# Kernel optimization log

Hardware: AMD Instinct MI355X
Metric: run time of the kernel (lower is better)

The kernel has to match this reference:

```python
import jax, jax.numpy as jnp
import numpy as np

V, D, T, H, L, B = 50257, 1024, 1024, 16, 6, 2
HS = D // H  # 64
EPS = 1e-5


def setup_inputs() -> dict:
    key = jax.random.key(0)
    ks = jax.random.split(key, 16)
    s = 0.02
    n = lambda k, sh: jax.random.normal(k, sh, jnp.float32) * s
    return {
        'idx': jax.random.randint(ks[0], (B, T), 0, V),
        'targets': jax.random.randint(ks[1], (B, T), 0, V),
        'tok_emb': n(ks[2], (V, D)),
        'pos_emb': n(ks[3], (T, D)),
        'wq': n(ks[4], (L, H, D, HS)),
        'wk': n(ks[5], (L, H, D, HS)),
        'wv': n(ks[6], (L, H, D, HS)),
        'wproj': n(ks[7], (L, D, D)),
        'bproj': jnp.zeros((L, D), jnp.float32),
        'ln1_g': jnp.ones((L, D), jnp.float32),
        'ln1_b': jnp.zeros((L, D), jnp.float32),
        'ln2_g': jnp.ones((L, D), jnp.float32),
        'ln2_b': jnp.zeros((L, D), jnp.float32),
        'w1': n(ks[8], (L, D, 4 * D)),
        'b1': jnp.zeros((L, 4 * D), jnp.float32),
        'w2': n(ks[9], (L, 4 * D, D)),
        'b2': jnp.zeros((L, D), jnp.float32),
        'lnf_g': jnp.ones((D,), jnp.float32),
        'lnf_b': jnp.zeros((D,), jnp.float32),
        'lm_w': n(ks[10], (D, V)),
        'lm_b': jnp.zeros((V,), jnp.float32),
    }


def _layernorm(x, g, b):
    mu = jnp.mean(x, axis=-1, keepdims=True)
    var = jnp.var(x, axis=-1, keepdims=True)
    return (x - mu) * jax.lax.rsqrt(var + EPS) * g + b


def _forward(idx, targets, tok_emb, pos_emb, wq, wk, wv, wproj, bproj,
             ln1_g, ln1_b, ln2_g, ln2_b, w1, b1, w2, b2, lnf_g, lnf_b, lm_w, lm_b):
    t = idx.shape[1]
    x = tok_emb[idx] + pos_emb[:t]  # [B,T,D]
    causal = jnp.tril(jnp.ones((t, t), bool))  # [T,T]
    neg_inf = jnp.float32(-jnp.inf)

    def block(x, p):
        (wq_l, wk_l, wv_l, wp_l, bp_l, g1, b1_ln, g2, b2_ln, wf1, bf1, wf2, bf2) = p
        h = _layernorm(x, g1, b1_ln)
        q = jnp.einsum('btd,hdk->bhtk', h, wq_l)
        k = jnp.einsum('btd,hdk->bhtk', h, wk_l)
        v = jnp.einsum('btd,hdk->bhtk', h, wv_l)
        scores = jnp.einsum('bhtk,bhsk->bhts', q, k) * (HS ** -0.5)
        scores = jnp.where(causal, scores, neg_inf)
        attn = jax.nn.softmax(scores, axis=-1)  # dropout p=0.0
        o = jnp.einsum('bhts,bhsk->bhtk', attn, v)
        o = o.transpose(0, 2, 1, 3).reshape(x.shape[0], t, H * HS)  # concat heads
        x = x + o @ wp_l + bp_l
        h2 = _layernorm(x, g2, b2_ln)
        x = x + jax.nn.relu(h2 @ wf1 + bf1) @ wf2 + bf2
        return x, None

    x, _ = jax.lax.scan(block, x, (wq, wk, wv, wproj, bproj,
                                   ln1_g, ln1_b, ln2_g, ln2_b, w1, b1, w2, b2))
    x = _layernorm(x, lnf_g, lnf_b)
    logits = x @ lm_w + lm_b  # [B,T,V]
    logp = jax.nn.log_softmax(logits, axis=-1)
    loss = -jnp.mean(jnp.take_along_axis(logp, targets[..., None], axis=-1))
    return logits, loss


def reference(idx, targets, tok_emb, pos_emb, wq, wk, wv, wproj, bproj,
              ln1_g, ln1_b, ln2_g, ln2_b, w1, b1, w2, b2, lnf_g, lnf_b, lm_w, lm_b):
    return _forward(idx, targets, tok_emb, pos_emb, wq, wk, wv, wproj, bproj,
                    ln1_g, ln1_b, ln2_g, ln2_b, w1, b1, w2, b2, lnf_g, lnf_b, lm_w, lm_b)
```

## Files before the change

kernel.cpp:

```cpp
#include <hip/hip_runtime.h>
#include <cstdint>
#include <cstddef>

typedef unsigned short u16;
typedef unsigned int u32;
typedef __bf16 bf16x8 __attribute__((ext_vector_type(8)));
typedef float f32x4 __attribute__((ext_vector_type(4)));
typedef short short8_t __attribute__((ext_vector_type(8)));

#define NV 50257
#define NVPAD 50304
#define ND 1024
#define NT 1024
#define NH 16
#define NL 6
#define NB 2
#define NM 2048
#define NF 4096
#define EPSLN 1e-5f

__device__ __forceinline__ u16 f2bf(float f) {
    unsigned u = __float_as_uint(f);
    return (u16)((u + 0x7fffu + ((u >> 16) & 1u)) >> 16);
}
__device__ __forceinline__ float bf2f(u16 h) {
    return __uint_as_float(((unsigned)h) << 16);
}
__device__ __forceinline__ u32 pack2bf(float lo, float hi) {
    return (u32)f2bf(lo) | ((u32)f2bf(hi) << 16);
}

__device__ __forceinline__ void gload_lds16(const u16* g, u16* l) {
    __builtin_amdgcn_global_load_lds((const __attribute__((address_space(1))) void*)g,
                                     (__attribute__((address_space(3))) void*)l, 16, 0, 0);
}

__device__ __forceinline__ float wave_reduce_sum(float v) {
#pragma unroll
    for (int off = 32; off >= 1; off >>= 1) v += __shfl_xor(v, off, 64);
    return v;
}

__global__ __launch_bounds__(256) void k_embed(const int* __restrict__ idx,
                                               const float* __restrict__ tok,
                                               const float* __restrict__ pos,
                                               float* __restrict__ x) {
    int m = blockIdx.x;
    int t = m & (NT - 1);
    int tokid = idx[m];
    int d = threadIdx.x * 4;
    float4 a = *(const float4*)(tok + (size_t)tokid * ND + d);
    float4 p = *(const float4*)(pos + (size_t)t * ND + d);
    a.x += p.x; a.y += p.y; a.z += p.z; a.w += p.w;
    *(float4*)(x + (size_t)m * ND + d) = a;
}

__global__ __launch_bounds__(256) void k_layernorm(const float* __restrict__ x,
                                                   const float* __restrict__ g,
                                                   const float* __restrict__ b,
                                                   u16* __restrict__ outb) {
    int m = blockIdx.x;
    int d = threadIdx.x * 4;
    const float4 v = *(const float4*)(x + (size_t)m * ND + d);
    float s = v.x + v.y + v.z + v.w;
    float q = v.x * v.x + v.y * v.y + v.z * v.z + v.w * v.w;
    s = wave_reduce_sum(s);
    q = wave_reduce_sum(q);
    __shared__ float ss[4], sq[4];
    int lane = threadIdx.x & 63, w = threadIdx.x >> 6;
    if (lane == 0) { ss[w] = s; sq[w] = q; }
    __syncthreads();
    s = ss[0] + ss[1] + ss[2] + ss[3];
    q = sq[0] + sq[1] + sq[2] + sq[3];
    float mu = s * (1.0f / ND);
    float var = q * (1.0f / ND) - mu * mu;
    float rstd = rsqrtf(var + EPSLN);
    float4 gg = *(const float4*)(g + d);
    float4 bb = *(const float4*)(b + d);
    ushort4 pk;
    pk.x = f2bf((v.x - mu) * rstd * gg.x + bb.x);
    pk.y = f2bf((v.y - mu) * rstd * gg.y + bb.y);
    pk.z = f2bf((v.z - mu) * rstd * gg.z + bb.z);
    pk.w = f2bf((v.w - mu) * rstd * gg.w + bb.w);
    *(ushort4*)(outb + (size_t)m * ND + d) = pk;
}

__global__ __launch_bounds__(256) void k_wtrans(const float* __restrict__ W,
                                                u16* __restrict__ Wt,
                                                int K, int N, int Npad, int hs, int ld) {
    __shared__ float t[32][33];
    const int nb = blockIdx.x << 5, kb = blockIdx.y << 5;
    const int tx = threadIdx.x & 31, tq = threadIdx.x >> 5;
    const int n = nb + tx;
    if (n < N) {
        const int head = n / hs, nc = n - head * hs;
        const float* src = W + (size_t)head * K * hs + nc;
#pragma unroll
        for (int i = 0; i < 4; ++i)
            t[(tq << 2) + i][tx] = src[(size_t)(kb + (tq << 2) + i) * ld];
    } else {
#pragma unroll
        for (int i = 0; i < 4; ++i) t[(tq << 2) + i][tx] = 0.f;
    }
    __syncthreads();
#pragma unroll
    for (int i = 0; i < 4; ++i) {
        const int nn = nb + (tq << 2) + i;
        if (nn < Npad) Wt[(size_t)nn * K + kb + tx] = f2bf(t[tx][(tq << 2) + i]);
    }
}

__global__ __launch_bounds__(256) void k_wtrans_qkv(const float* __restrict__ Wq,
                                                    const float* __restrict__ Wk,
                                                    const float* __restrict__ Wv,
                                                    u16* __restrict__ Wt) {
    __shared__ float t[32][33];
    const float* W = (blockIdx.z == 0) ? Wq : (blockIdx.z == 1) ? Wk : Wv;
    u16* dst = Wt + (size_t)blockIdx.z * ND * ND;
    const int nb = blockIdx.x << 5, kb = blockIdx.y << 5;
    const int tx = threadIdx.x & 31, tq = threadIdx.x >> 5;
    const int n = nb + tx;
    {
        const int head = n >> 6, nc = n & 63;
        const float* src = W + (size_t)head * ND * 64 + nc;
#pragma unroll
        for (int i = 0; i < 4; ++i)
            t[(tq << 2) + i][tx] = src[(size_t)(kb + (tq << 2) + i) * 64];
    }
    __syncthreads();
#pragma unroll
    for (int i = 0; i < 4; ++i) {
        const int nn = nb + (tq << 2) + i;
        dst[(size_t)nn * ND + kb + tx] = f2bf(t[tx][(tq << 2) + i]);
    }
}

__global__ __launch_bounds__(256) void k_vtrans(const u16* __restrict__ qkv,
                                                u16* __restrict__ vt) {
    __shared__ u16 L[64][72];
    const int tt = blockIdx.x, bh = blockIdx.y;
    const int b = bh >> 4, h = bh & 15;
    const int tid = threadIdx.x;
    const int tr = tid >> 2, dc = (tid & 3) << 4;
    const u16* src = qkv + (size_t)(b * NT + tt * 64 + tr) * 3072 + 2048 + h * 64 + dc;
    short8_t v0 = *(const short8_t*)src;
    short8_t v1 = *(const short8_t*)(src + 8);
#pragma unroll
    for (int j = 0; j < 8; ++j) { L[tr][dc + j] = (u16)v0[j]; L[tr][dc + 8 + j] = (u16)v1[j]; }
    __syncthreads();
    const int dr = tid >> 2, tc = (tid & 3) << 4;
    union { u16 us[16]; short8_t v[2]; } tmp;
#pragma unroll
    for (int j = 0; j < 16; ++j) tmp.us[j] = L[tc + j][dr];
    u16* dst = vt + ((size_t)bh * 64 + dr) * NT + tt * 64 + tc;
    *(short8_t*)dst = tmp.v[0];
    *(short8_t*)(dst + 8) = tmp.v[1];
}

__global__ __launch_bounds__(512) void k_gemm_lm(
    const u16* __restrict__ A, const u16* __restrict__ Bt,
    const float* __restrict__ bias,
    float* __restrict__ Cf,
    int K, int N, int ldc)
{
    __shared__ u16 As[2][256 * 32];
    __shared__ u16 Bs[2][128 * 32];
    const int lin = blockIdx.y * 8 + blockIdx.x;
    const int nwg = (int)gridDim.y * 8;
    const int cpx = nwg >> 3;
    const int swz = (lin & 7) * cpx + (lin >> 3);
    const int m0 = (swz & 7) * 256;
    const int n0 = (swz >> 3) * 128;
    const int tid = threadIdx.x;
    const int lane = tid & 63, w = tid >> 6;
    const int wr = w >> 1, wc = w & 1;
    const int lr = lane & 15, kg = lane >> 4;

    const int srow = lane >> 2;
    const int scol = (((lane & 3) ^ ((lane >> 3) & 3)) << 3);
    const u16* gA0 = A + (size_t)(m0 + w * 16 + srow) * K + scol;
    const u16* gA1 = gA0 + (size_t)128 * K;
    const u16* gB0 = Bt + (size_t)(n0 + w * 16 + srow) * K + scol;

    f32x4 acc[4][4] = {};
    const int nt = K >> 5;

    gload_lds16(gA0, &As[0][w * 512]);
    gload_lds16(gA1, &As[0][4096 + w * 512]);
    gload_lds16(gB0, &Bs[0][w * 512]);
    __syncthreads();

    int cur = 0;
    for (int t = 0; t < nt; ++t) {
        if (t + 1 < nt) {
            const int ko = (t + 1) << 5;
            gload_lds16(gA0 + ko, &As[cur ^ 1][w * 512]);
            gload_lds16(gA1 + ko, &As[cur ^ 1][4096 + w * 512]);
            gload_lds16(gB0 + ko, &Bs[cur ^ 1][w * 512]);
        }
        bf16x8 af[4], bfr[4];
        const int rsw = ((kg ^ ((lr >> 1) & 3)) << 3);
#pragma unroll
        for (int mi = 0; mi < 4; ++mi)
            af[mi] = *(const bf16x8*)&As[cur][(wr * 64 + mi * 16 + lr) * 32 + rsw];
#pragma unroll
        for (int ni = 0; ni < 4; ++ni)
            bfr[ni] = *(const bf16x8*)&Bs[cur][(wc * 64 + ni * 16 + lr) * 32 + rsw];
#pragma unroll
        for (int mi = 0; mi < 4; ++mi)
#pragma unroll
            for (int ni = 0; ni < 4; ++ni)
                acc[mi][ni] = __builtin_amdgcn_mfma_f32_16x16x32_bf16(af[mi], bfr[ni], acc[mi][ni], 0, 0, 0);
        __syncthreads();
        cur ^= 1;
    }
#pragma unroll
    for (int mi = 0; mi < 4; ++mi)
#pragma unroll
        for (int ni = 0; ni < 4; ++ni)
#pragma unroll
            for (int r = 0; r < 4; ++r) {
                const int row = m0 + wr * 64 + mi * 16 + kg * 4 + r;
                const int col = n0 + wc * 64 + ni * 16 + lr;
                if (col >= N) continue;
                Cf[(size_t)row * ldc + col] = acc[mi][ni][r] + bias[col];
            }
}

template <bool RELU, bool NBOUND, bool OUTBF16>
__global__ __launch_bounds__(256) void k_mfma_gemm(
    const u16* __restrict__ A, const u16* __restrict__ Bt,
    const float* __restrict__ bias,
    float* __restrict__ Cf, u16* __restrict__ Cb,
    int K, int N, int ldc)
{
    __shared__ u16 As[2][128 * 32];
    __shared__ u16 Bs[2][128 * 32];
    const int lin = blockIdx.y * 16 + blockIdx.x;
    const int nwg = (int)gridDim.y * 16;
    const int cpx = nwg >> 3;
    const int swz = (lin & 7) * cpx + (lin >> 3);
    const int m0 = (swz & 15) * 128;
    const int n0 = (swz >> 4) * 128;
    const int tid = threadIdx.x;
    const int lane = tid & 63, wv = tid >> 6;
    const int wr = wv >> 1, wc = wv & 1;
    const int lr = lane & 15, kg = lane >> 4;

    const int srow = lane >> 2;
    const int scol = (((lane & 3) ^ ((lane >> 3) & 3)) << 3);
    const u16* gA0 = A + (size_t)(m0 + wv * 16 + srow) * K + scol;
    const u16* gA1 = gA0 + (size_t)64 * K;
    const u16* gB0 = Bt + (size_t)(n0 + wv * 16 + srow) * K + scol;
    const u16* gB1 = gB0 + (size_t)64 * K;

    f32x4 acc[4][4] = {};
    const int nt = K >> 5;

    gload_lds16(gA0, &As[0][wv * 512]);
    gload_lds16(gA1, &As[0][2048 + wv * 512]);
    gload_lds16(gB0, &Bs[0][wv * 512]);
    gload_lds16(gB1, &Bs[0][2048 + wv * 512]);
    __syncthreads();

    int cur = 0;
    for (int t = 0; t < nt; ++t) {
        if (t + 1 < nt) {
            const int ko = (t + 1) << 5;
            gload_lds16(gA0 + ko, &As[cur ^ 1][wv * 512]);
            gload_lds16(gA1 + ko, &As[cur ^ 1][2048 + wv * 512]);
            gload_lds16(gB0 + ko, &Bs[cur ^ 1][wv * 512]);
            gload_lds16(gB1 + ko, &Bs[cur ^ 1][2048 + wv * 512]);
        }
        bf16x8 af[4], bfr[4];
        const int rsw = ((kg ^ ((lr >> 1) & 3)) << 3);
#pragma unroll
        for (int mi = 0; mi < 4; ++mi) {
            const int R = wr * 64 + mi * 16 + lr;
            af[mi] = *(const bf16x8*)&As[cur][R * 32 + rsw];
        }
#pragma unroll
        for (int ni = 0; ni < 4; ++ni) {
            const int R = wc * 64 + ni * 16 + lr;
            bfr[ni] = *(const bf16x8*)&Bs[cur][R * 32 + rsw];
        }
#pragma unroll
        for (int mi = 0; mi < 4; ++mi)
#pragma unroll
            for (int ni = 0; ni < 4; ++ni)
                acc[mi][ni] = __builtin_amdgcn_mfma_f32_16x16x32_bf16(af[mi], bfr[ni], acc[mi][ni], 0, 0, 0);
        __syncthreads();
        cur ^= 1;
    }
#pragma unroll
    for (int mi = 0; mi < 4; ++mi) {
#pragma unroll
        for (int ni = 0; ni < 4; ++ni) {
#pragma unroll
            for (int r = 0; r < 4; ++r) {
                const int row = m0 + wr * 64 + mi * 16 + kg * 4 + r;
                const int col = n0 + wc * 64 + ni * 16 + lr;
                if (NBOUND && col >= N) continue;
                float c = acc[mi][ni][r];
                if (bias) c += bias[col];
                if (RELU) c = fmaxf(c, 0.f);
                if (OUTBF16) Cb[(size_t)row * ldc + col] = f2bf(c);
                else         Cf[(size_t)row * ldc + col] = c;
            }
        }
    }
}

template <bool RELU, bool RESID, bool OUTBF16>
__global__ __launch_bounds__(256) void k_gemm_n64(
    const u16* __restrict__ A, const u16* __restrict__ Bt,
    const float* __restrict__ bias, const float* __restrict__ resid,
    float* __restrict__ Cf, u16* __restrict__ Cb,
    int K, int ldc)
{
    __shared__ u16 As[2][128 * 32];
    __shared__ u16 Bs[2][64 * 32];
    const int lin = blockIdx.y * 16 + blockIdx.x;
    const int nwg = (int)gridDim.y * 16;
    const int cpx = nwg >> 3;
    const int swz = (lin & 7) * cpx + (lin >> 3);
    const int m0 = (swz & 15) * 128;
    const int n0 = (swz >> 4) * 64;
    const int tid = threadIdx.x;
    const int lane = tid & 63, wv = tid >> 6;
    const int lr = lane & 15, kg = lane >> 4;

    const int srow = lane >> 2;
    const int scol = (((lane & 3) ^ ((lane >> 3) & 3)) << 3);
    const u16* gA0 = A + (size_t)(m0 + wv * 32 + srow) * K + scol;
    const u16* gA1 = gA0 + (size_t)16 * K;
    const u16* gB0 = Bt + (size_t)(n0 + wv * 16 + srow) * K + scol;

    f32x4 acc[2][4] = {};
    const int nt = K >> 5;

    gload_lds16(gA0, &As[0][wv * 1024]);
    gload_lds16(gA1, &As[0][wv * 1024 + 512]);
    gload_lds16(gB0, &Bs[0][wv * 512]);
    __syncthreads();

    int cur = 0;
    for (int t = 0; t < nt; ++t) {
        if (t + 1 < nt) {
            const int ko = (t + 1) << 5;
            gload_lds16(gA0 + ko, &As[cur ^ 1][wv * 1024]);
            gload_lds16(gA1 + ko, &As[cur ^ 1][wv * 1024 + 512]);
            gload_lds16(gB0 + ko, &Bs[cur ^ 1][wv * 512]);
        }
        bf16x8 af[2], bfr[4];
        const int rsw = ((kg ^ ((lr >> 1) & 3)) << 3);
#pragma unroll
        for (int mi = 0; mi < 2; ++mi)
            af[mi] = *(const bf16x8*)&As[cur][(wv * 32 + mi * 16 + lr) * 32 + rsw];
#pragma unroll
        for (int ni = 0; ni < 4; ++ni)
            bfr[ni] = *(const bf16x8*)&Bs[cur][(ni * 16 + lr) * 32 + rsw];
#pragma unroll
        for (int mi = 0; mi < 2; ++mi)
#pragma unroll
            for (int ni = 0; ni < 4; ++ni)
                acc[mi][ni] = __builtin_amdgcn_mfma_f32_16x16x32_bf16(af[mi], bfr[ni], acc[mi][ni], 0, 0, 0);
        __syncthreads();
        cur ^= 1;
    }
#pragma unroll
    for (int mi = 0; mi < 2; ++mi) {
#pragma unroll
        for (int ni = 0; ni < 4; ++ni) {
#pragma unroll
            for (int r = 0; r < 4; ++r) {
                const int row = m0 + wv * 32 + mi * 16 + kg * 4 + r;
                const int col = n0 + ni * 16 + lr;
                float c = acc[mi][ni][r];
                if (bias) c += bias[col];
                if (RELU) c = fmaxf(c, 0.f);
                if (RESID) c += resid[(size_t)row * ldc + col];
                if (OUTBF16) Cb[(size_t)row * ldc + col] = f2bf(c);
                else         Cf[(size_t)row * ldc + col] = c;
            }
        }
    }
}

__global__ __launch_bounds__(256) void k_attn_mfma(const u16* __restrict__ qkv,
                                                   const u16* __restrict__ vt,
                                                   u16* __restrict__ ob) {
    const int qt = blockIdx.x, bh = blockIdx.y;
    const int b = bh >> 4, h = bh & 15;
    const int tid = threadIdx.x;
    const int lane = tid & 63, w = tid >> 6;
    const int lr = lane & 15, kg = lane >> 4;

    __shared__ u16 Qs[64 * 64];
    __shared__ u16 Ks[2][64 * 64];
    __shared__ u16 Vs[2][64 * 64];

    const int srow8 = lane >> 3;
    const int csw = ((lane & 7) ^ srow8) << 3;

    {
        const int r0 = w * 8 + srow8;
        gload_lds16(qkv + (size_t)(b * NT + qt * 64 + r0) * 3072 + h * 64 + csw, &Qs[w * 512]);
        gload_lds16(qkv + (size_t)(b * NT + qt * 64 + 32 + r0) * 3072 + h * 64 + csw, &Qs[2048 + w * 512]);
    }
#define STAGE_KV(bb, st)                                                                            \
    {                                                                                               \
        const int r0_ = w * 8 + srow8;                                                              \
        gload_lds16(qkv + (size_t)(b * NT + (st) * 64 + r0_) * 3072 + 1024 + h * 64 + csw,          \
                    &Ks[bb][w * 512]);                                                              \
        gload_lds16(qkv + (size_t)(b * NT + (st) * 64 + 32 + r0_) * 3072 + 1024 + h * 64 + csw,     \
                    &Ks[bb][2048 + w * 512]);                                                       \
        gload_lds16(vt + ((size_t)bh * 64 + r0_) * NT + (st) * 64 + csw, &Vs[bb][w * 512]);         \
        gload_lds16(vt + ((size_t)bh * 64 + 32 + r0_) * NT + (st) * 64 + csw,                       \
                    &Vs[bb][2048 + w * 512]);                                                       \
    }
    STAGE_KV(0, 0);
    __syncthreads();

    bf16x8 qf[2];
    {
        const int qrow = w * 16 + lr;
#pragma unroll
        for (int ds_ = 0; ds_ < 2; ++ds_)
            qf[ds_] = *(const bf16x8*)&Qs[qrow * 64 + ((((ds_ << 2) + kg) ^ (lr & 7)) << 3)];
    }

    float mstate = -3.0e38f, lstate = 0.f;
    f32x4 acc_o[4] = {};
    const int qg = qt * 64 + w * 16 + lr;

    int cur = 0;
    for (int st = 0; st <= qt; ++st) {
        if (st < qt) STAGE_KV(cur ^ 1, st + 1);
        const bool diag = (st == qt);
        const int milim = diag ? w : 3;

        f32x4 acc_s[4] = {};
#pragma unroll
        for (int mi = 0; mi < 4; ++mi) {
            if (mi <= milim) {
                const int srw = mi * 16 + lr;
#pragma unroll
                for (int ds_ = 0; ds_ < 2; ++ds_) {
                    bf16x8 kf = *(const bf16x8*)&Ks[cur][srw * 64 + ((((ds_ << 2) + kg) ^ (lr & 7)) << 3)];
                    acc_s[mi] = __builtin_amdgcn_mfma_f32_16x16x32_bf16(kf, qf[ds_], acc_s[mi], 0, 0, 0);
                }
            }
        }
        float tilemax = -3.0e38f;
#pragma unroll
        for (int mi = 0; mi < 4; ++mi)
#pragma unroll
            for (int r = 0; r < 4; ++r) {
                float x_ = acc_s[mi][r] * 0.125f;
                const int sg = st * 64 + mi * 16 + kg * 4 + r;
                if (mi > milim || sg > qg) x_ = -3.0e38f;
                acc_s[mi][r] = x_;
                tilemax = fmaxf(tilemax, x_);
            }
        tilemax = fmaxf(tilemax, __shfl_xor(tilemax, 16));
        tilemax = fmaxf(tilemax, __shfl_xor(tilemax, 32));
        const float mnew = fmaxf(mstate, tilemax);
        const float rfac = __expf(mstate - mnew);
        mstate = mnew;

        float psum = 0.f;
        u32 pk[4][2];
#pragma unroll
        for (int mi = 0; mi < 4; ++mi) {
            float p0 = __expf(acc_s[mi][0] - mnew);
            float p1 = __expf(acc_s[mi][1] - mnew);
            float p2 = __expf(acc_s[mi][2] - mnew);
            float p3 = __expf(acc_s[mi][3] - mnew);
            psum += p0 + p1 + p2 + p3;
            pk[mi][0] = pack2bf(p0, p1);
            pk[mi][1] = pack2bf(p2, p3);
        }
        psum += __shfl_xor(psum, 16);
        psum += __shfl_xor(psum, 32);
        lstate = lstate * rfac + psum;

        float rf[4];
#pragma unroll
        for (int r = 0; r < 4; ++r) rf[r] = __shfl(rfac, kg * 4 + r);
#pragma unroll
        for (int ni = 0; ni < 4; ++ni)
#pragma unroll
            for (int r = 0; r < 4; ++r) acc_o[ni][r] *= rf[r];

        const int src0 = ((kg & 1) << 5) + lr;
        const int src1 = src0 + 16;
#pragma unroll
        for (int ks_ = 0; ks_ < 2; ++ks_) {
            const u32 lo_a = __shfl((int)pk[ks_ * 2][0], src0);
            const u32 lo_b = __shfl((int)pk[ks_ * 2][1], src0);
            const u32 lo_c = __shfl((int)pk[ks_ * 2][0], src1);
            const u32 lo_d = __shfl((int)pk[ks_ * 2][1], src1);
            const u32 hi_a = __shfl((int)pk[ks_ * 2 + 1][0], src0);
            const u32 hi_b = __shfl((int)pk[ks_ * 2 + 1][1], src0);
            const u32 hi_c = __shfl((int)pk[ks_ * 2 + 1][0], src1);
            const u32 hi_d = __shfl((int)pk[ks_ * 2 + 1][1], src1);
            union { u32 u[4]; bf16x8 v; } pa;
            pa.u[0] = (kg & 2) ? hi_a : lo_a;
            pa.u[1] = (kg & 2) ? hi_b : lo_b;
            pa.u[2] = (kg & 2) ? hi_c : lo_c;
            pa.u[3] = (kg & 2) ? hi_d : lo_d;
#pragma unroll
            for (int ni = 0; ni < 4; ++ni) {
                const int drow = ni * 16 + lr;
                bf16x8 vf = *(const bf16x8*)&Vs[cur][drow * 64 + ((((ks_ << 2) + kg) ^ (lr & 7)) << 3)];
                acc_o[ni] = __builtin_amdgcn_mfma_f32_16x16x32_bf16(pa.v, vf, acc_o[ni], 0, 0, 0);
            }
        }
        __syncthreads();
        cur ^= 1;
    }

    float il[4];
#pragma unroll
    for (int r = 0; r < 4; ++r) il[r] = 1.0f / __shfl(lstate, kg * 4 + r);
#pragma unroll
    for (int ni = 0; ni < 4; ++ni)
#pragma unroll
        for (int r = 0; r < 4; ++r) {
            const int q2 = qt * 64 + w * 16 + kg * 4 + r;
            ob[(size_t)(b * NT + q2) * ND + h * 64 + ni * 16 + lr] = f2bf(acc_o[ni][r] * il[r]);
        }
#undef STAGE_KV
}

__global__ __launch_bounds__(256) void k_rowloss(const float* __restrict__ logits,
                                                 const int* __restrict__ targets,
                                                 float* __restrict__ rl) {
    const int m = blockIdx.x;
    const float* row = logits + (size_t)m * NV;
    const int tid = threadIdx.x;
    const int lane = tid & 63, w = tid >> 6;
    const int a = (4 - (m & 3)) & 3;
    const float4* rv = (const float4*)(row + a);
    const int nv4 = (NV - a) >> 2;
    const int tail0 = a + (nv4 << 2);

    float mx = -INFINITY;
    if (tid < a) mx = row[tid];
    for (int j = tid; j < nv4; j += 256) {
        float4 v = rv[j];
        mx = fmaxf(fmaxf(mx, v.x), fmaxf(v.y, fmaxf(v.z, v.w)));
    }
    for (int j = tail0 + tid; j < NV; j += 256) mx = fmaxf(mx, row[j]);
#pragma unroll
    for (int off = 32; off >= 1; off >>= 1) mx = fmaxf(mx, __shfl_xor(mx, off, 64));
    __shared__ float sm[4];
    if (lane == 0) sm[w] = mx;
    __syncthreads();
    mx = fmaxf(fmaxf(sm[0], sm[1]), fmaxf(sm[2], sm[3]));

    float s = 0.f;
    if (tid < a) s += __expf(row[tid] - mx);
    for (int j = tid; j < nv4; j += 256) {
        float4 v = rv[j];
        s += __expf(v.x - mx) + __expf(v.y - mx) + __expf(v.z - mx) + __expf(v.w - mx);
    }
    for (int j = tail0 + tid; j < NV; j += 256) s += __expf(row[j] - mx);
    s = wave_reduce_sum(s);
    __shared__ float sv[4];
    if (lane == 0) sv[w] = s;
    __syncthreads();
    s = sv[0] + sv[1] + sv[2] + sv[3];
    if (tid == 0) {
        float lse = logf(s) + mx;
        rl[m] = lse - row[targets[m]];
    }
}

__global__ __launch_bounds__(256) void k_lossreduce(const float* __restrict__ rl,
                                                    float* __restrict__ out_loss) {
    int tid = threadIdx.x;
    float s = 0.f;
    for (int j = tid; j < NM; j += 256) s += rl[j];
    s = wave_reduce_sum(s);
    __shared__ float sv[4];
    int lane = tid & 63, w = tid >> 6;
    if (lane == 0) sv[w] = s;
    __syncthreads();
    if (tid == 0) out_loss[0] = (sv[0] + sv[1] + sv[2] + sv[3]) * (1.0f / NM);
}

extern "C" void kernel_launch(void* const* d_in, const int* in_sizes, int n_in,
                              void* d_out, int out_size, void* d_ws, size_t ws_size,
                              hipStream_t stream) {
    const int* idx      = (const int*)d_in[0];
    const int* targets  = (const int*)d_in[1];
    const float* tok    = (const float*)d_in[2];
    const float* pos    = (const float*)d_in[3];
    const float* wq     = (const float*)d_in[4];
    const float* wk     = (const float*)d_in[5];
    const float* wv     = (const float*)d_in[6];
    const float* wproj  = (const float*)d_in[7];
    const float* bproj  = (const float*)d_in[8];
    const float* ln1_g  = (const float*)d_in[9];
    const float* ln1_b  = (const float*)d_in[10];
    const float* ln2_g  = (const float*)d_in[11];
    const float* ln2_b  = (const float*)d_in[12];
    const float* w1     = (const float*)d_in[13];
    const float* b1     = (const float*)d_in[14];
    const float* w2     = (const float*)d_in[15];
    const float* b2     = (const float*)d_in[16];
    const float* lnf_g  = (const float*)d_in[17];
    const float* lnf_b  = (const float*)d_in[18];
    const float* lm_w   = (const float*)d_in[19];
    const float* lm_b   = (const float*)d_in[20];
    float* out = (float*)d_out;

    char* wsb = (char*)d_ws;
    auto alloc = [&](size_t bytes) { char* p = wsb; wsb += (bytes + 255) & ~(size_t)255; return p; };
    float* x     = (float*)alloc((size_t)NM * ND * 4);
    u16* h_bf    = (u16*)  alloc((size_t)NM * ND * 2);
    float* rl    = (float*)alloc((size_t)NM * 4);
    char* region = (char*)alloc((size_t)NVPAD * ND * 2);
    u16* qkv_bf = (u16*)(region);
    u16* vt_bf  = (u16*)(region + ((size_t)12 << 20));
    u16* ob_bf  = (u16*)(region + ((size_t)16 << 20));
    u16* hid_bf = (u16*)(region + ((size_t)20 << 20));
    u16* wqkv_t = (u16*)(region + ((size_t)36 << 20));
    u16* wp_t   = (u16*)(region + ((size_t)42 << 20));
    u16* w1_t   = (u16*)(region + ((size_t)44 << 20));
    u16* w2_t   = (u16*)(region + ((size_t)52 << 20));
    u16* lm_t   = (u16*)(region);

    k_embed<<<NM, 256, 0, stream>>>(idx, tok, pos, x);

    for (int l = 0; l < NL; ++l) {
        const float* wq_l = wq + (size_t)l * NH * ND * 64;
        const float* wk_l = wk + (size_t)l * NH * ND * 64;
        const float* wv_l = wv + (size_t)l * NH * ND * 64;
        const float* wp_l = wproj + (size_t)l * ND * ND;
        const float* bp_l = bproj + (size_t)l * ND;
        const float* w1_l = w1 + (size_t)l * ND * NF;
        const float* b1_l = b1 + (size_t)l * NF;
        const float* w2_l = w2 + (size_t)l * NF * ND;
        const float* b2_l = b2 + (size_t)l * ND;

        k_layernorm<<<NM, 256, 0, stream>>>(x, ln1_g + (size_t)l * ND, ln1_b + (size_t)l * ND, h_bf);

        k_wtrans_qkv<<<dim3(32, 32, 3), 256, 0, stream>>>(wq_l, wk_l, wv_l, wqkv_t);
        k_mfma_gemm<false, false, true><<<dim3(16, 24), 256, 0, stream>>>(
            h_bf, wqkv_t, nullptr, nullptr, qkv_bf, ND, 3 * ND, 3 * ND);

        k_vtrans<<<dim3(NT / 64, NB * NH), 256, 0, stream>>>(qkv_bf, vt_bf);
        k_attn_mfma<<<dim3(NT / 64, NB * NH), 256, 0, stream>>>(qkv_bf, vt_bf, ob_bf);

        k_wtrans<<<dim3(ND / 32, ND / 32), 256, 0, stream>>>(wp_l, wp_t, ND, ND, ND, ND, ND);
        k_gemm_n64<false, true, false><<<dim3(16, 16), 256, 0, stream>>>(
            ob_bf, wp_t, bp_l, x, x, nullptr, ND, ND);

        k_layernorm<<<NM, 256, 0, stream>>>(x, ln2_g + (size_t)l * ND, ln2_b + (size_t)l * ND, h_bf);

        k_wtrans<<<dim3(NF / 32, ND / 32), 256, 0, stream>>>(w1_l, w1_t, ND, NF, NF, NF, NF);
        k_mfma_gemm<true, false, true><<<dim3(16, 32), 256, 0, stream>>>(
            h_bf, w1_t, b1_l, nullptr, hid_bf, ND, NF, NF);

        k_wtrans<<<dim3(ND / 32, NF / 32), 256, 0, stream>>>(w2_l, w2_t, NF, ND, ND, ND, ND);
        k_gemm_n64<false, true, false><<<dim3(16, 16), 256, 0, stream>>>(
            hid_bf, w2_t, b2_l, x, x, nullptr, NF, ND);
    }

    k_layernorm<<<NM, 256, 0, stream>>>(x, lnf_g, lnf_b, h_bf);

    k_wtrans<<<dim3(NVPAD / 32, ND / 32), 256, 0, stream>>>(lm_w, lm_t, ND, NV, NVPAD, NV, NV);
    k_gemm_lm<<<dim3(8, NVPAD / 128), 512, 0, stream>>>(
        h_bf, lm_t, lm_b, out, ND, NV, NV);

    k_rowloss<<<NM, 256, 0, stream>>>(out, targets, rl);
    k_lossreduce<<<1, 256, 0, stream>>>(rl, out + (size_t)NM * NV);
}
```

Baseline: 1.894 ms.

## Fuse softmax partials into LM GEMM, split-K the FFN down-projection, reorder attention blocks

The LM-head GEMM epilogue now computes a per-row max and sum-exp for each 128-column tile and writes them to small partial buffers. A light combine kernel reduces these to the loss, so the 400MB logits tensor is no longer reread in a separate row-loss pass. The FFN down-projection is split into two K halves written to a scratch buffer, then summed with bias and residual in a combine kernel, which raises the block count at the cost of extra traffic. Attention reverses the query-tile order for the second batch to balance causal work across blocks.

New measurement: 1.663 ms. 12.2% less time.

```diff
diff --git a/kernel.cpp b/kernel.cpp
--- a/kernel.cpp
+++ b/kernel.cpp
@@ -10,6 +10,7 @@
 
 #define NV 50257
 #define NVPAD 50304
+#define NBLK_LM 393
 #define ND 1024
 #define NT 1024
 #define NH 16
@@ -161,6 +162,7 @@
     const u16* __restrict__ A, const u16* __restrict__ Bt,
     const float* __restrict__ bias,
     float* __restrict__ Cf,
+    float* __restrict__ pmax_g, float* __restrict__ psum_g,
     int K, int N, int ldc)
 {
     __shared__ u16 As[2][256 * 32];
@@ -214,6 +216,7 @@
         __syncthreads();
         cur ^= 1;
     }
+
 #pragma unroll
     for (int mi = 0; mi < 4; ++mi)
 #pragma unroll
@@ -223,8 +226,55 @@
                 const int row = m0 + wr * 64 + mi * 16 + kg * 4 + r;
                 const int col = n0 + wc * 64 + ni * 16 + lr;
                 if (col >= N) continue;
-                Cf[(size_t)row * ldc + col] = acc[mi][ni][r] + bias[col];
+                acc[mi][ni][r] += bias[col];
+                Cf[(size_t)row * ldc + col] = acc[mi][ni][r];
             }
+
+    float* redm = (float*)As;
+    float* reds = redm + 512;
+#pragma unroll
+    for (int mi = 0; mi < 4; ++mi)
+#pragma unroll
+        for (int r = 0; r < 4; ++r) {
+            float vmax = -3.0e38f;
+#pragma unroll
+            for (int ni = 0; ni < 4; ++ni) {
+                const int col = n0 + wc * 64 + ni * 16 + lr;
+                vmax = fmaxf(vmax, (col < N) ? acc[mi][ni][r] : -3.0e38f);
+            }
+            vmax = fmaxf(vmax, __shfl_xor(vmax, 1));
+            vmax = fmaxf(vmax, __shfl_xor(vmax, 2));
+            vmax = fmaxf(vmax, __shfl_xor(vmax, 4));
+            vmax = fmaxf(vmax, __shfl_xor(vmax, 8));
+            if (lr == 0) redm[wc * 256 + wr * 64 + mi * 16 + kg * 4 + r] = vmax;
+        }
+    __syncthreads();
+#pragma unroll
+    for (int mi = 0; mi < 4; ++mi)
+#pragma unroll
+        for (int r = 0; r < 4; ++r) {
+            const int rloc = wr * 64 + mi * 16 + kg * 4 + r;
+            const float M = fmaxf(redm[rloc], redm[256 + rloc]);
+            float s = 0.f;
+#pragma unroll
+            for (int ni = 0; ni < 4; ++ni) {
+                const int col = n0 + wc * 64 + ni * 16 + lr;
+                if (col < N) s += __expf(acc[mi][ni][r] - M);
+            }
+            s += __shfl_xor(s, 1);
+            s += __shfl_xor(s, 2);
+            s += __shfl_xor(s, 4);
+            s += __shfl_xor(s, 8);
+            if (lr == 0) reds[wc * 256 + rloc] = s;
+        }
+    __syncthreads();
+    if (tid < 256) {
+        const float M = fmaxf(redm[tid], redm[256 + tid]);
+        const float S = reds[tid] + reds[256 + tid];
+        const int nblk = n0 >> 7;
+        pmax_g[(size_t)nblk * NM + m0 + tid] = M;
+        psum_g[(size_t)nblk * NM + m0 + tid] = S;
+    }
 }
 
 template <bool RELU, bool NBOUND, bool OUTBF16>
@@ -311,6 +361,100 @@
     }
 }
 
+__global__ __launch_bounds__(256) void k_gemm_ksplit(
+    const u16* __restrict__ A, const u16* __restrict__ Bt,
+    float* __restrict__ P,
+    int Khalf, int Ktot, int ldc)
+{
+    __shared__ u16 As[2][128 * 32];
+    __shared__ u16 Bs[2][128 * 32];
+    const int z = blockIdx.z;
+    const int lin = blockIdx.y * 16 + blockIdx.x;
+    const int nwg = (int)gridDim.y * 16;
+    const int cpx = nwg >> 3;
+    const int swz = (lin & 7) * cpx + (lin >> 3);
+    const int m0 = (swz & 15) * 128;
+    const int n0 = (swz >> 4) * 128;
+    const int tid = threadIdx.x;
+    const int lane = tid & 63, wv = tid >> 6;
+    const int wr = wv >> 1, wc = wv & 1;
+    const int lr = lane & 15, kg = lane >> 4;
+
+    const int srow = lane >> 2;
+    const int scol = (((lane & 3) ^ ((lane >> 3) & 3)) << 3);
+    const int koff = z * Khalf;
+    const u16* gA0 = A + (size_t)(m0 + wv * 16 + srow) * Ktot + koff + scol;
+    const u16* gA1 = gA0 + (size_t)64 * Ktot;
+    const u16* gB0 = Bt + (size_t)(n0 + wv * 16 + srow) * Ktot + koff + scol;
+    const u16* gB1 = gB0 + (size_t)64 * Ktot;
+    float* Pz = P + (size_t)z * NM * ldc;
+
+    f32x4 acc[4][4] = {};
+    const int nt = Khalf >> 5;
+
+    gload_lds16(gA0, &As[0][wv * 512]);
+    gload_lds16(gA1, &As[0][2048 + wv * 512]);
+    gload_lds16(gB0, &Bs[0][wv * 512]);
+    gload_lds16(gB1, &Bs[0][2048 + wv * 512]);
+    __syncthreads();
+
+    int cur = 0;
+    for (int t = 0; t < nt; ++t) {
+        if (t + 1 < nt) {
+            const int ko = (t + 1) << 5;
+            gload_lds16(gA0 + ko, &As[cur ^ 1][wv * 512]);
+            gload_lds16(gA1 + ko, &As[cur ^ 1][2048 + wv * 512]);
+            gload_lds16(gB0 + ko, &Bs[cur ^ 1][wv * 512]);
+            gload_lds16(gB1 + ko, &Bs[cur ^ 1][2048 + wv * 512]);
+        }
+        bf16x8 af[4], bfr[4];
+        const int rsw = ((kg ^ ((lr >> 1) & 3)) << 3);
+#pragma unroll
+        for (int mi = 0; mi < 4; ++mi) {
+            const int R = wr * 64 + mi * 16 + lr;
+            af[mi] = *(const bf16x8*)&As[cur][R * 32 + rsw];
+        }
+#pragma unroll
+        for (int ni = 0; ni < 4; ++ni) {
+            const int R = wc * 64 + ni * 16 + lr;
+            bfr[ni] = *(const bf16x8*)&Bs[cur][R * 32 + rsw];
+        }
+#pragma unroll
+        for (int mi = 0; mi < 4; ++mi)
+#pragma unroll
+            for (int ni = 0; ni < 4; ++ni)
+                acc[mi][ni] = __builtin_amdgcn_mfma_f32_16x16x32_bf16(af[mi], bfr[ni], acc[mi][ni], 0, 0, 0);
+        __syncthreads();
+        cur ^= 1;
+    }
+#pragma unroll
+    for (int mi = 0; mi < 4; ++mi)
+#pragma unroll
+        for (int ni = 0; ni < 4; ++ni)
+#pragma unroll
+            for (int r = 0; r < 4; ++r) {
+                const int row = m0 + wr * 64 + mi * 16 + kg * 4 + r;
+                const int col = n0 + wc * 64 + ni * 16 + lr;
+                Pz[(size_t)row * ldc + col] = acc[mi][ni][r];
+            }
+}
+
+__global__ __launch_bounds__(256) void k_combine(const float* __restrict__ p,
+                                                 const float* __restrict__ bias,
+                                                 float* __restrict__ x) {
+    const int m = blockIdx.x;
+    const int d = threadIdx.x * 4;
+    float4 a  = *(const float4*)(x + (size_t)m * ND + d);
+    float4 q0 = *(const float4*)(p + (size_t)m * ND + d);
+    float4 q1 = *(const float4*)(p + (size_t)NM * ND + (size_t)m * ND + d);
+    float4 bb = *(const float4*)(bias + d);
+    a.x += q0.x + q1.x + bb.x;
+    a.y += q0.y + q1.y + bb.y;
+    a.z += q0.z + q1.z + bb.z;
+    a.w += q0.w + q1.w + bb.w;
+    *(float4*)(x + (size_t)m * ND + d) = a;
+}
+
 template <bool RELU, bool RESID, bool OUTBF16>
 __global__ __launch_bounds__(256) void k_gemm_n64(
     const u16* __restrict__ A, const u16* __restrict__ Bt,
@@ -390,7 +534,8 @@
 __global__ __launch_bounds__(256) void k_attn_mfma(const u16* __restrict__ qkv,
                                                    const u16* __restrict__ vt,
                                                    u16* __restrict__ ob) {
-    const int qt = blockIdx.x, bh = blockIdx.y;
+    const int qt = (blockIdx.y < 16) ? (int)blockIdx.x : 15 - (int)blockIdx.x;
+    const int bh = blockIdx.y;
     const int b = bh >> 4, h = bh & 15;
     const int tid = threadIdx.x;
     const int lane = tid & 63, w = tid >> 6;
@@ -534,48 +679,23 @@
 #undef STAGE_KV
 }
 
-__global__ __launch_bounds__(256) void k_rowloss(const float* __restrict__ logits,
-                                                 const int* __restrict__ targets,
-                                                 float* __restrict__ rl) {
-    const int m = blockIdx.x;
-    const float* row = logits + (size_t)m * NV;
-    const int tid = threadIdx.x;
-    const int lane = tid & 63, w = tid >> 6;
-    const int a = (4 - (m & 3)) & 3;
-    const float4* rv = (const float4*)(row + a);
-    const int nv4 = (NV - a) >> 2;
-    const int tail0 = a + (nv4 << 2);
-
-    float mx = -INFINITY;
-    if (tid < a) mx = row[tid];
-    for (int j = tid; j < nv4; j += 256) {
-        float4 v = rv[j];
-        mx = fmaxf(fmaxf(mx, v.x), fmaxf(v.y, fmaxf(v.z, v.w)));
-    }
-    for (int j = tail0 + tid; j < NV; j += 256) mx = fmaxf(mx, row[j]);
-#pragma unroll
-    for (int off = 32; off >= 1; off >>= 1) mx = fmaxf(mx, __shfl_xor(mx, off, 64));
-    __shared__ float sm[4];
-    if (lane == 0) sm[w] = mx;
-    __syncthreads();
-    mx = fmaxf(fmaxf(sm[0], sm[1]), fmaxf(sm[2], sm[3]));
-
-    float s = 0.f;
-    if (tid < a) s += __expf(row[tid] - mx);
-    for (int j = tid; j < nv4; j += 256) {
-        float4 v = rv[j];
-        s += __expf(v.x - mx) + __expf(v.y - mx) + __expf(v.z - mx) + __expf(v.w - mx);
-    }
-    for (int j = tail0 + tid; j < NV; j += 256) s += __expf(row[j] - mx);
-    s = wave_reduce_sum(s);
-    __shared__ float sv[4];
-    if (lane == 0) sv[w] = s;
-    __syncthreads();
-    s = sv[0] + sv[1] + sv[2] + sv[3];
-    if (tid == 0) {
-        float lse = logf(s) + mx;
-        rl[m] = lse - row[targets[m]];
-    }
+__global__ __launch_bounds__(256) void k_losscombine(const float* __restrict__ pmax,
+                                                     const float* __restrict__ psum,
+                                                     const float* __restrict__ logits,
+                                                     const int* __restrict__ targets,
+                                                     float* __restrict__ rl) {
+    const int row = blockIdx.x * 4 + (threadIdx.x >> 6);
+    const int lane = threadIdx.x & 63;
+    float M = -3.0e38f;
+    for (int j = lane; j < NBLK_LM; j += 64) M = fmaxf(M, pmax[(size_t)j * NM + row]);
+#pragma unroll
+    for (int off = 32; off >= 1; off >>= 1) M = fmaxf(M, __shfl_xor(M, off, 64));
+    float S = 0.f;
+    for (int j = lane; j < NBLK_LM; j += 64)
+        S += psum[(size_t)j * NM + row] * __expf(pmax[(size_t)j * NM + row] - M);
+    S = wave_reduce_sum(S);
+    if (lane == 0)
+        rl[row] = M + logf(S) - logits[(size_t)row * NV + targets[row]];
 }
 
 __global__ __launch_bounds__(256) void k_lossreduce(const float* __restrict__ rl,
@@ -622,6 +742,8 @@
     float* x     = (float*)alloc((size_t)NM * ND * 4);
     u16* h_bf    = (u16*)  alloc((size_t)NM * ND * 2);
     float* rl    = (float*)alloc((size_t)NM * 4);
+    float* pmax  = (float*)alloc((size_t)NBLK_LM * NM * 4);
+    float* psum  = (float*)alloc((size_t)NBLK_LM * NM * 4);
     char* region = (char*)alloc((size_t)NVPAD * ND * 2);
     u16* qkv_bf = (u16*)(region);
     u16* vt_bf  = (u16*)(region + ((size_t)12 << 20));
@@ -631,6 +753,7 @@
     u16* wp_t   = (u16*)(region + ((size_t)42 << 20));
     u16* w1_t   = (u16*)(region + ((size_t)44 << 20));
     u16* w2_t   = (u16*)(region + ((size_t)52 << 20));
+    float* p01  = (float*)(region + ((size_t)60 << 20));
     u16* lm_t   = (u16*)(region);
 
     k_embed<<<NM, 256, 0, stream>>>(idx, tok, pos, x);
@@ -666,16 +789,17 @@
             h_bf, w1_t, b1_l, nullptr, hid_bf, ND, NF, NF);
 
         k_wtrans<<<dim3(ND / 32, NF / 32), 256, 0, stream>>>(w2_l, w2_t, NF, ND, ND, ND, ND);
-        k_gemm_n64<false, true, false><<<dim3(16, 16), 256, 0, stream>>>(
-            hid_bf, w2_t, b2_l, x, x, nullptr, NF, ND);
+        k_gemm_ksplit<<<dim3(16, 8, 2), 256, 0, stream>>>(
+            hid_bf, w2_t, p01, NF / 2, NF, ND);
+        k_combine<<<NM, 256, 0, stream>>>(p01, b2_l, x);
     }
 
     k_layernorm<<<NM, 256, 0, stream>>>(x, lnf_g, lnf_b, h_bf);
 
     k_wtrans<<<dim3(NVPAD / 32, ND / 32), 256, 0, stream>>>(lm_w, lm_t, ND, NV, NVPAD, NV, NV);
     k_gemm_lm<<<dim3(8, NVPAD / 128), 512, 0, stream>>>(
-        h_bf, lm_t, lm_b, out, ND, NV, NV);
-
-    k_rowloss<<<NM, 256, 0, stream>>>(out, targets, rl);
+        h_bf, lm_t, lm_b, out, pmax, psum, ND, NV, NV);
+
+    k_losscombine<<<NM / 4, 256, 0, stream>>>(pmax, psum, out, targets, rl);
     k_lossreduce<<<1, 256, 0, stream>>>(rl, out + (size_t)NM * NV);
 }
```
